# Optimization experiments

Measured on AMD Instinct MI355X. Metric: run time of the kernel, lower is better.

## Reference

```python
import jax, jax.numpy as jnp
import numpy as np
from jax import lax

B, C, H, W = 4, 256, 32, 32   # latent: NCHW, C == codebook embed dim
N_CODES = 16384


def setup_inputs() -> dict:
    key = jax.random.key(0)
    k1, k2, k3 = jax.random.split(key, 3)
    latent = jax.random.normal(k1, (B, C, H, W), jnp.float32)
    codebook = jax.random.normal(k2, (N_CODES, C), jnp.float32)
    dec_w = jax.random.normal(k3, (3, C, 3, 3), jnp.float32) * 0.02
    dec_b = jnp.zeros((3,), jnp.float32)
    return {"latent": latent, "codebook": codebook, "dec_w": dec_w, "dec_b": dec_b}


def vector_quantize(x, codebook):
    # x: [B,H,W,D], codebook: [N,D]. Squared-L2 nearest neighbor + gather,
    # straight-through gradient (replace_grad(x_q, x)).
    d = ((x * x).sum(-1, keepdims=True)
         - 2.0 * jnp.einsum('bhwd,nd->bhwn', x, codebook)
         + (codebook * codebook).sum(-1))          # [B,H,W,N]
    idx = jnp.argmin(d, axis=-1)                    # [B,H,W]
    x_q = codebook[idx]                             # gather -> [B,H,W,D]
    return x + lax.stop_gradient(x_q - x)


@jax.custom_vjp
def clamp_with_grad(x):
    return jnp.clip(x, 0.0, 1.0)

def _cwg_fwd(x):
    return jnp.clip(x, 0.0, 1.0), x

def _cwg_bwd(x, g):
    # pass gradient only where it points back toward the valid range
    keep = (g * (x - jnp.clip(x, 0.0, 1.0)) >= 0).astype(g.dtype)
    return (g * keep,)

clamp_with_grad.defvjp(_cwg_fwd, _cwg_bwd)


def decode(quant, dec_w, dec_b):
    # stub VQGAN decoder: single 3x3 conv embed_dim -> 3 (NCHW)
    y = lax.conv_general_dilated(quant, dec_w, window_strides=(1, 1),
                                 padding='SAME',
                                 dimension_numbers=('NCHW', 'OIHW', 'NCHW'))
    return y + dec_b[None, :, None, None]


def reference(latent, codebook, dec_w, dec_b):
    x = jnp.moveaxis(latent, 1, 3)                  # NCHW -> NHWC
    quant = jnp.moveaxis(vector_quantize(x, codebook), 3, 1)  # back to NCHW
    img = decode(quant, dec_w, dec_b)
    return clamp_with_grad((img + 1.0) * 0.5)
```

## Files before the change

kernel.cpp:

```cpp
#include <hip/hip_runtime.h>
#include <hip/hip_bf16.h>
#include <stdint.h>

#define P_TOT   4096
#define N_CODE  16384
#define DIM     256
#define HW      1024
#define CHW     262144
#define NBLK    64

typedef unsigned long long u64;
typedef unsigned short u16;
typedef __attribute__((ext_vector_type(4))) float f32x4;
typedef __attribute__((ext_vector_type(8))) short bf16x8;
typedef __attribute__((ext_vector_type(8))) unsigned short ushort8;

#define FENCE() asm volatile("" ::: "memory")
#define BAR()   __builtin_amdgcn_s_barrier()
#define VM(n)   asm volatile("s_waitcnt vmcnt(" #n ")" ::: "memory")

__device__ __forceinline__ unsigned int mono(float f) {
  unsigned int u = __float_as_uint(f);
  return (u & 0x80000000u) ? ~u : (u | 0x80000000u);
}
__device__ __forceinline__ u16 f2bf(float f) {
  __hip_bfloat16 h = __float2bfloat16(f);
  return *(u16*)&h;
}
__device__ __forceinline__ float bf2f(u16 b) {
  __hip_bfloat16 h = *(__hip_bfloat16*)&b;
  return __bfloat162float(h);
}
__device__ __forceinline__ void gload16(const void* g, void* l) {
  __builtin_amdgcn_global_load_lds(
      (const __attribute__((address_space(1))) unsigned int*)g,
      (__attribute__((address_space(3))) unsigned int*)l, 16, 0, 0);
}

__global__ __launch_bounds__(256) void k_split_cb(const float* __restrict__ cb,
                                                  u16* __restrict__ bfrag) {
  __shared__ float ls[64][68];
  int blk = blockIdx.x;
  int kp = blk & 3, bq = (blk >> 2) & 3, nb = blk >> 4;
  int t = threadIdx.x;
  int code0 = nb * 256 + bq * 64;
  int k0 = kp * 64;
  int lr = t >> 4, lc = (t & 15) * 4;
  #pragma unroll
  for (int pss = 0; pss < 4; ++pss) {
    int row = pss * 16 + lr;
    float4 v = *(const float4*)&cb[(size_t)(code0 + row) * DIM + k0 + lc];
    ls[row][lc] = v.x; ls[row][lc + 1] = v.y; ls[row][lc + 2] = v.z; ls[row][lc + 3] = v.w;
  }
  __syncthreads();
  int row64 = t & 63, g = t >> 6;
  #pragma unroll
  for (int it = 0; it < 4; ++it) {
    int combo = it * 4 + g;
    int kt2 = combo >> 3, s = (combo >> 1) & 3, h = combo & 1;
    int kt = kp * 2 + kt2;
    ushort8 o;
    #pragma unroll
    for (int e = 0; e < 8; ++e) {
      float x = ls[row64][kt2 * 32 + s * 8 + e];
      u16 hi = f2bf(x);
      o[e] = h ? f2bf(x - bf2f(hi)) : hi;
    }
    size_t unitIdx = (size_t)(nb * 8 + kt) * 4 + bq;
    *(ushort8*)&bfrag[unitIdx * 4096 + (size_t)((h * 4 + s) * 64 + row64) * 8] = o;
  }
}

__global__ __launch_bounds__(256) void k_split_x(const float* __restrict__ latent,
                                                 u16* __restrict__ xfrag) {
  __shared__ float ls[256][68];
  int blk = blockIdx.x;
  int aq = blk & 3, mb = blk >> 2;
  int t = threadIdx.x;
  int gp0 = mb * 256 + aq * 64;
  int b = gp0 >> 10, hw0 = gp0 & 1023;
  int hw = t & 63, cg = t >> 6;
  for (int pss = 0; pss < 64; ++pss) {
    int c = pss * 4 + cg;
    ls[c][hw] = latent[(size_t)b * CHW + (size_t)c * HW + hw0 + hw];
  }
  __syncthreads();
  int row64 = t & 63, g = t >> 6;
  #pragma unroll
  for (int it = 0; it < 16; ++it) {
    int combo = it * 4 + g;
    int kt = combo >> 3, s = (combo >> 1) & 3, h = combo & 1;
    ushort8 o;
    #pragma unroll
    for (int e = 0; e < 8; ++e) {
      float x = ls[kt * 32 + s * 8 + e][row64];
      u16 hi = f2bf(x);
      o[e] = h ? f2bf(x - bf2f(hi)) : hi;
    }
    size_t unitIdx = (size_t)(mb * 8 + kt) * 4 + aq;
    *(ushort8*)&xfrag[unitIdx * 4096 + (size_t)((h * 4 + s) * 64 + row64) * 8] = o;
  }
}

__global__ __launch_bounds__(256) void k_cnorm(const float* __restrict__ cb,
                                               float* __restrict__ cnorm) {
  int code = blockIdx.x * 4 + (threadIdx.x >> 6);
  int lane = threadIdx.x & 63;
  float4 v = ((const float4*)(cb + (size_t)code * DIM))[lane];
  float s = fmaf(v.x, v.x, fmaf(v.y, v.y, fmaf(v.z, v.z, v.w * v.w)));
  #pragma unroll
  for (int off = 32; off; off >>= 1) s += __shfl_down(s, off, 64);
  if (lane == 0) cnorm[code] = s;
}

__global__ __launch_bounds__(256) void k_wt(const float* __restrict__ w,
                                            float* __restrict__ wt) {
  int e = blockIdx.x * 256 + threadIdx.x;
  int ic = e & 255;
  int r = e >> 8;
  int kx = r % 3; r /= 3;
  int ky = r % 3;
  int oc = r / 3;
  wt[e] = w[((oc * 256 + ic) * 3 + ky) * 3 + kx];
}

__global__ __launch_bounds__(512, 2) void k_vq(const u16* __restrict__ xfrag,
                                               const u16* __restrict__ bfrag,
                                               const float* __restrict__ cnorm,
                                               u64* __restrict__ partial) {
  __shared__ u16 lds[2][2][4][4096];

  int bid = blockIdx.x;
  int wg = (bid & 7) * 128 + (bid >> 3);
  int nb = wg >> 4;
  int mb = wg & 15;

  int tid = threadIdx.x;
  int lane = tid & 63, w = tid >> 6;
  int fr = lane & 15, s = lane >> 4;
  int aq = w >> 1;
  int rbase = (w & 1) * 32;
  int tid8 = tid * 8;

  const u16* Xb = xfrag + (size_t)mb * 32 * 4096;
  const u16* Bb = bfrag + (size_t)nb * 32 * 4096;

  f32x4 acc[2][16] = {};
  bf16x8 ah[2], al[2], bh[4], bl[4];

  #pragma unroll
  for (int r = 0; r < 4; ++r) gload16(Xb + (size_t)r * 4096 + tid8, &lds[0][0][r][0] + tid8);
  #pragma unroll
  for (int r = 0; r < 4; ++r) gload16(Bb + (size_t)r * 4096 + tid8, &lds[0][1][r][0] + tid8);
  VM(3);
  BAR(); FENCE();

  #define READ_A(LA)                                                          \
    _Pragma("unroll")                                                         \
    for (int m = 0; m < 2; ++m) {                                             \
      ah[m] = *(const bf16x8*)&(LA)[aq * 4096 + (size_t)((0 + s) * 64 + rbase + m * 16 + fr) * 8]; \
      al[m] = *(const bf16x8*)&(LA)[aq * 4096 + (size_t)((4 + s) * 64 + rbase + m * 16 + fr) * 8]; \
    }
  #define READ_B(LB, q)                                                       \
    _Pragma("unroll")                                                         \
    for (int j = 0; j < 4; ++j) {                                             \
      bh[j] = *(const bf16x8*)&(LB)[(q) * 4096 + (size_t)((0 + s) * 64 + j * 16 + fr) * 8]; \
      bl[j] = *(const bf16x8*)&(LB)[(q) * 4096 + (size_t)((4 + s) * 64 + j * 16 + fr) * 8]; \
    }
  #define MFMAQ(q)                                                            \
    __builtin_amdgcn_s_setprio(1);                                            \
    _Pragma("unroll")                                                         \
    for (int m = 0; m < 2; ++m) {                                             \
      _Pragma("unroll")                                                       \
      for (int j = 0; j < 4; ++j)                                             \
        acc[m][(q) * 4 + j] = __builtin_amdgcn_mfma_f32_16x16x32_bf16(ah[m], bh[j], acc[m][(q) * 4 + j], 0, 0, 0); \
    }                                                                         \
    _Pragma("unroll")                                                         \
    for (int m = 0; m < 2; ++m) {                                             \
      _Pragma("unroll")                                                       \
      for (int j = 0; j < 4; ++j)                                             \
        acc[m][(q) * 4 + j] = __builtin_amdgcn_mfma_f32_16x16x32_bf16(ah[m], bl[j], acc[m][(q) * 4 + j], 0, 0, 0); \
    }                                                                         \
    _Pragma("unroll")                                                         \
    for (int m = 0; m < 2; ++m) {                                             \
      _Pragma("unroll")                                                       \
      for (int j = 0; j < 4; ++j)                                             \
        acc[m][(q) * 4 + j] = __builtin_amdgcn_mfma_f32_16x16x32_bf16(al[m], bh[j], acc[m][(q) * 4 + j], 0, 0, 0); \
    }                                                                         \
    __builtin_amdgcn_s_setprio(0);

  for (int t = 0; t < 7; ++t) {
    const int cur = t & 1, nxt = cur ^ 1;
    u16* LA = &lds[cur][0][0][0];
    u16* LB = &lds[cur][1][0][0];
    const size_t u1 = (size_t)(t + 1) * 4;
    READ_A(LA); READ_B(LB, 0);
    gload16(Xb + (u1 + 0) * 4096 + tid8, &lds[nxt][0][0][0] + tid8);
    gload16(Xb + (u1 + 1) * 4096 + tid8, &lds[nxt][0][1][0] + tid8);
    BAR();
    MFMAQ(0);
    VM(4); BAR(); FENCE();
    READ_B(LB, 1);
    gload16(Xb + (u1 + 2) * 4096 + tid8, &lds[nxt][0][2][0] + tid8);
    gload16(Xb + (u1 + 3) * 4096 + tid8, &lds[nxt][0][3][0] + tid8);
    BAR();
    MFMAQ(1);
    VM(5); BAR(); FENCE();
    READ_B(LB, 2);
    gload16(Bb + (u1 + 0) * 4096 + tid8, &lds[nxt][1][0][0] + tid8);
    gload16(Bb + (u1 + 1) * 4096 + tid8, &lds[nxt][1][1][0] + tid8);
    BAR();
    MFMAQ(2);
    VM(6); BAR(); FENCE();
    READ_B(LB, 3);
    gload16(Bb + (u1 + 2) * 4096 + tid8, &lds[nxt][1][2][0] + tid8);
    gload16(Bb + (u1 + 3) * 4096 + tid8, &lds[nxt][1][3][0] + tid8);
    BAR();
    MFMAQ(3);
    VM(3); BAR(); FENCE();
  }
  {
    u16* LA = &lds[1][0][0][0];
    u16* LB = &lds[1][1][0][0];
    READ_A(LA); READ_B(LB, 0);
    BAR(); MFMAQ(0); VM(2); BAR(); FENCE();
    READ_B(LB, 1);
    BAR(); MFMAQ(1); VM(1); BAR(); FENCE();
    READ_B(LB, 2);
    BAR(); MFMAQ(2); VM(0); BAR(); FENCE();
    READ_B(LB, 3);
    BAR(); MFMAQ(3);
  }

  float cnr[16];
  #pragma unroll
  for (int n = 0; n < 16; ++n) cnr[n] = cnorm[nb * 256 + n * 16 + fr];

  #pragma unroll
  for (int m = 0; m < 2; ++m) {
    u64 best[4];
    #pragma unroll
    for (int r = 0; r < 4; ++r) best[r] = ~0ull;
    #pragma unroll
    for (int n = 0; n < 16; ++n) {
      unsigned code = (unsigned)(nb * 256 + n * 16 + fr);
      #pragma unroll
      for (int r = 0; r < 4; ++r) {
        float val = fmaf(-2.0f, acc[m][n][r], cnr[n]);
        u64 key = ((u64)mono(val) << 32) | code;
        if (key < best[r]) best[r] = key;
      }
    }
    #pragma unroll
    for (int d = 1; d < 16; d <<= 1) {
      #pragma unroll
      for (int r = 0; r < 4; ++r) {
        u64 o = __shfl_xor(best[r], d, 64);
        if (o < best[r]) best[r] = o;
      }
    }
    if (fr == 0) {
      int rowb = mb * 256 + w * 32 + m * 16 + s * 4;
      #pragma unroll
      for (int r = 0; r < 4; ++r)
        partial[(size_t)(rowb + r) * NBLK + nb] = best[r];
    }
  }
}

__global__ __launch_bounds__(64) void k_reduce(const u64* __restrict__ partial,
                                               const float* __restrict__ latent,
                                               const float* __restrict__ cb,
                                               int* __restrict__ idxo) {
  int p = blockIdx.x;
  int t = threadIdx.x;
  u64 v = partial[(size_t)p * NBLK + t];
  u64 m1 = v;
  #pragma unroll
  for (int d = 1; d < 64; d <<= 1) { u64 o = __shfl_xor(m1, d, 64); if (o < m1) m1 = o; }
  u64 vv = (v == m1) ? ~0ull : v;
  u64 m2 = vv;
  #pragma unroll
  for (int d = 1; d < 64; d <<= 1) { u64 o = __shfl_xor(m2, d, 64); if (o < m2) m2 = o; }
  int n1 = (int)(m1 & 0xFFFFFFFFull);
  int n2 = (int)(m2 & 0xFFFFFFFFull);

  int b = p >> 10, hw = p & 1023;
  const float* xb = latent + (size_t)b * CHW + hw;
  double d1 = 0.0, d2 = 0.0;
  #pragma unroll
  for (int q = 0; q < 4; ++q) {
    int c = t * 4 + q;
    double xv = (double)xb[(size_t)c * HW];
    double e1 = xv - (double)cb[(size_t)n1 * DIM + c]; d1 += e1 * e1;
    double e2 = xv - (double)cb[(size_t)n2 * DIM + c]; d2 += e2 * e2;
  }
  #pragma unroll
  for (int d = 32; d; d >>= 1) {
    d1 += __shfl_down(d1, d, 64);
    d2 += __shfl_down(d2, d, 64);
  }
  if (t == 0) {
    idxo[p] = (d2 < d1 || (d2 == d1 && n2 < n1)) ? n2 : n1;
  }
}

__global__ __launch_bounds__(256) void k_conv(const float* __restrict__ cb,
                                              const int* __restrict__ idx,
                                              const float* __restrict__ wt,
                                              const float* __restrict__ bias,
                                              float* __restrict__ out) {
  int y = blockIdx.x, b = blockIdx.y;
  int t = threadIdx.x;
  int x = t & 31, icg = t >> 5;
  float a0 = 0.f, a1 = 0.f, a2 = 0.f;
  #pragma unroll
  for (int dy = -1; dy <= 1; dy++) {
    int yy = y + dy;
    if (yy < 0 || yy >= 32) continue;
    #pragma unroll
    for (int dx = -1; dx <= 1; dx++) {
      int xx = x + dx;
      if (xx < 0 || xx >= 32) continue;
      int n = idx[b * HW + yy * 32 + xx];
      const float4* crow = (const float4*)(cb + (size_t)n * DIM + icg * 32);
      int tap = (dy + 1) * 3 + (dx + 1);
      const float4* w0 = (const float4*)(wt + (size_t)(0 * 9 + tap) * DIM + icg * 32);
      const float4* w1 = (const float4*)(wt + (size_t)(1 * 9 + tap) * DIM + icg * 32);
      const float4* w2 = (const float4*)(wt + (size_t)(2 * 9 + tap) * DIM + icg * 32);
      #pragma unroll
      for (int q = 0; q < 8; q++) {
        float4 qv = crow[q];
        float4 wa = w0[q];
        a0 = fmaf(qv.x, wa.x, a0); a0 = fmaf(qv.y, wa.y, a0);
        a0 = fmaf(qv.z, wa.z, a0); a0 = fmaf(qv.w, wa.w, a0);
        float4 wb = w1[q];
        a1 = fmaf(qv.x, wb.x, a1); a1 = fmaf(qv.y, wb.y, a1);
        a1 = fmaf(qv.z, wb.z, a1); a1 = fmaf(qv.w, wb.w, a1);
        float4 wcv = w2[q];
        a2 = fmaf(qv.x, wcv.x, a2); a2 = fmaf(qv.y, wcv.y, a2);
        a2 = fmaf(qv.z, wcv.z, a2); a2 = fmaf(qv.w, wcv.w, a2);
      }
    }
  }
  __shared__ float red[3][32][8];
  red[0][x][icg] = a0; red[1][x][icg] = a1; red[2][x][icg] = a2;
  __syncthreads();
  if (t < 96) {
    int oc = t >> 5, xo = t & 31;
    float sum = 0.f;
    #pragma unroll
    for (int k = 0; k < 8; k++) sum += red[oc][xo][k];
    sum += bias[oc];
    sum = (sum + 1.0f) * 0.5f;
    sum = fminf(fmaxf(sum, 0.0f), 1.0f);
    out[((size_t)(b * 3 + oc) * 32 + y) * 32 + xo] = sum;
  }
}

extern "C" void kernel_launch(void* const* d_in, const int* in_sizes, int n_in,
                              void* d_out, int out_size, void* d_ws, size_t ws_size,
                              hipStream_t stream) {
  const float* latent = (const float*)d_in[0];
  const float* cb     = (const float*)d_in[1];
  const float* dec_w  = (const float*)d_in[2];
  const float* dec_b  = (const float*)d_in[3];
  float* out = (float*)d_out;

  char* ws = (char*)d_ws;
  u64*   partial = (u64*)ws;
  float* cnorm   = (float*)(ws + 0x200000);
  int*   idx     = (int*)  (ws + 0x210000);
  float* wt      = (float*)(ws + 0x214000);
  u16*   xfrag   = (u16*)  (ws + 0x400000);
  u16*   bfrag   = (u16*)  (ws + 0x800000);

  k_split_cb<<<dim3(1024), dim3(256), 0, stream>>>(cb, bfrag);
  k_split_x <<<dim3(64),   dim3(256), 0, stream>>>(latent, xfrag);
  k_cnorm   <<<dim3(N_CODE / 4), dim3(256), 0, stream>>>(cb, cnorm);
  k_wt      <<<dim3(27),   dim3(256), 0, stream>>>(dec_w, wt);
  k_vq      <<<dim3(1024), dim3(512), 0, stream>>>(xfrag, bfrag, cnorm, partial);
  k_reduce  <<<dim3(P_TOT), dim3(64), 0, stream>>>(partial, latent, cb, idx);
  k_conv    <<<dim3(32, 4), dim3(256), 0, stream>>>(cb, idx, wt, dec_b, out);
}
```

Before: 203.7 us.

## Hold X fragments in registers, stream codebook only, and merge prep kernels

```diff
diff --git a/kernel.cpp b/kernel.cpp
--- a/kernel.cpp
+++ b/kernel.cpp
@@ -7,7 +7,7 @@
 #define DIM     256
 #define HW      1024
 #define CHW     262144
-#define NBLK    64
+#define NBLK    16
 
 typedef unsigned long long u64;
 typedef unsigned short u16;
@@ -37,234 +37,219 @@
       (__attribute__((address_space(3))) unsigned int*)l, 16, 0, 0);
 }
 
-__global__ __launch_bounds__(256) void k_split_cb(const float* __restrict__ cb,
-                                                  u16* __restrict__ bfrag) {
+__global__ __launch_bounds__(256) void k_prep(const float* __restrict__ cb,
+                                              const float* __restrict__ latent,
+                                              const float* __restrict__ dec_w,
+                                              u16* __restrict__ bfrag,
+                                              u16* __restrict__ xfrag,
+                                              float* __restrict__ cnorm,
+                                              float* __restrict__ wt) {
   __shared__ float ls[64][68];
-  int blk = blockIdx.x;
-  int kp = blk & 3, bq = (blk >> 2) & 3, nb = blk >> 4;
+  int bid = blockIdx.x;
   int t = threadIdx.x;
-  int code0 = nb * 256 + bq * 64;
-  int k0 = kp * 64;
-  int lr = t >> 4, lc = (t & 15) * 4;
-  #pragma unroll
-  for (int pss = 0; pss < 4; ++pss) {
-    int row = pss * 16 + lr;
-    float4 v = *(const float4*)&cb[(size_t)(code0 + row) * DIM + k0 + lc];
-    ls[row][lc] = v.x; ls[row][lc + 1] = v.y; ls[row][lc + 2] = v.z; ls[row][lc + 3] = v.w;
-  }
-  __syncthreads();
-  int row64 = t & 63, g = t >> 6;
-  #pragma unroll
-  for (int it = 0; it < 4; ++it) {
-    int combo = it * 4 + g;
-    int kt2 = combo >> 3, s = (combo >> 1) & 3, h = combo & 1;
-    int kt = kp * 2 + kt2;
-    ushort8 o;
-    #pragma unroll
-    for (int e = 0; e < 8; ++e) {
-      float x = ls[row64][kt2 * 32 + s * 8 + e];
-      u16 hi = f2bf(x);
-      o[e] = h ? f2bf(x - bf2f(hi)) : hi;
-    }
-    size_t unitIdx = (size_t)(nb * 8 + kt) * 4 + bq;
-    *(ushort8*)&bfrag[unitIdx * 4096 + (size_t)((h * 4 + s) * 64 + row64) * 8] = o;
-  }
-}
-
-__global__ __launch_bounds__(256) void k_split_x(const float* __restrict__ latent,
-                                                 u16* __restrict__ xfrag) {
-  __shared__ float ls[256][68];
-  int blk = blockIdx.x;
-  int aq = blk & 3, mb = blk >> 2;
-  int t = threadIdx.x;
-  int gp0 = mb * 256 + aq * 64;
-  int b = gp0 >> 10, hw0 = gp0 & 1023;
-  int hw = t & 63, cg = t >> 6;
-  for (int pss = 0; pss < 64; ++pss) {
-    int c = pss * 4 + cg;
-    ls[c][hw] = latent[(size_t)b * CHW + (size_t)c * HW + hw0 + hw];
-  }
-  __syncthreads();
-  int row64 = t & 63, g = t >> 6;
-  #pragma unroll
-  for (int it = 0; it < 16; ++it) {
-    int combo = it * 4 + g;
-    int kt = combo >> 3, s = (combo >> 1) & 3, h = combo & 1;
-    ushort8 o;
-    #pragma unroll
-    for (int e = 0; e < 8; ++e) {
-      float x = ls[kt * 32 + s * 8 + e][row64];
-      u16 hi = f2bf(x);
-      o[e] = h ? f2bf(x - bf2f(hi)) : hi;
-    }
-    size_t unitIdx = (size_t)(mb * 8 + kt) * 4 + aq;
-    *(ushort8*)&xfrag[unitIdx * 4096 + (size_t)((h * 4 + s) * 64 + row64) * 8] = o;
-  }
-}
-
-__global__ __launch_bounds__(256) void k_cnorm(const float* __restrict__ cb,
-                                               float* __restrict__ cnorm) {
-  int code = blockIdx.x * 4 + (threadIdx.x >> 6);
-  int lane = threadIdx.x & 63;
-  float4 v = ((const float4*)(cb + (size_t)code * DIM))[lane];
-  float s = fmaf(v.x, v.x, fmaf(v.y, v.y, fmaf(v.z, v.z, v.w * v.w)));
-  #pragma unroll
-  for (int off = 32; off; off >>= 1) s += __shfl_down(s, off, 64);
-  if (lane == 0) cnorm[code] = s;
-}
-
-__global__ __launch_bounds__(256) void k_wt(const float* __restrict__ w,
-                                            float* __restrict__ wt) {
-  int e = blockIdx.x * 256 + threadIdx.x;
-  int ic = e & 255;
-  int r = e >> 8;
-  int kx = r % 3; r /= 3;
-  int ky = r % 3;
-  int oc = r / 3;
-  wt[e] = w[((oc * 256 + ic) * 3 + ky) * 3 + kx];
-}
-
-__global__ __launch_bounds__(512, 2) void k_vq(const u16* __restrict__ xfrag,
+  if (bid < 1024) {
+    int blk = bid;
+    int kp = blk & 3, bq = (blk >> 2) & 3, nb = blk >> 4;
+    int code0 = nb * 256 + bq * 64;
+    int k0 = kp * 64;
+    int lr = t >> 4, lc = (t & 15) * 4;
+    #pragma unroll
+    for (int pss = 0; pss < 4; ++pss) {
+      int row = pss * 16 + lr;
+      float4 v = *(const float4*)&cb[(size_t)(code0 + row) * DIM + k0 + lc];
+      ls[row][lc] = v.x; ls[row][lc + 1] = v.y; ls[row][lc + 2] = v.z; ls[row][lc + 3] = v.w;
+    }
+    __syncthreads();
+    int row64 = t & 63, g = t >> 6;
+    #pragma unroll
+    for (int it = 0; it < 4; ++it) {
+      int combo = it * 4 + g;
+      int kt2 = combo >> 3, s = (combo >> 1) & 3, h = combo & 1;
+      int kt = kp * 2 + kt2;
+      ushort8 o;
+      #pragma unroll
+      for (int e = 0; e < 8; ++e) {
+        float x = ls[row64][kt2 * 32 + s * 8 + e];
+        u16 hi = f2bf(x);
+        o[e] = h ? f2bf(x - bf2f(hi)) : hi;
+      }
+      size_t unitIdx = (size_t)(nb * 8 + kt) * 4 + bq;
+      *(ushort8*)&bfrag[unitIdx * 4096 + (size_t)((h * 4 + s) * 64 + row64) * 8] = o;
+    }
+  } else if (bid < 1280) {
+    int blk = bid - 1024;
+    int kp = blk & 3, rowblk = blk >> 2;
+    int g0 = rowblk * 64;
+    int b = g0 >> 10, hw0 = g0 & 1023;
+    int c0 = kp * 64;
+    int ch = t >> 4, px4 = (t & 15) * 4;
+    #pragma unroll
+    for (int pss = 0; pss < 4; ++pss) {
+      int c = pss * 16 + ch;
+      float4 v = *(const float4*)&latent[(size_t)b * CHW + (size_t)(c0 + c) * HW + hw0 + px4];
+      ls[px4 + 0][c] = v.x; ls[px4 + 1][c] = v.y; ls[px4 + 2][c] = v.z; ls[px4 + 3][c] = v.w;
+    }
+    __syncthreads();
+    int row64 = t & 63, g = t >> 6;
+    #pragma unroll
+    for (int it = 0; it < 4; ++it) {
+      int combo = it * 4 + g;
+      int kt2 = combo >> 3, s = (combo >> 1) & 3, h = combo & 1;
+      int kt = kp * 2 + kt2;
+      ushort8 o;
+      #pragma unroll
+      for (int e = 0; e < 8; ++e) {
+        float x = ls[row64][kt2 * 32 + s * 8 + e];
+        u16 hi = f2bf(x);
+        o[e] = h ? f2bf(x - bf2f(hi)) : hi;
+      }
+      int mbO = rowblk >> 2, aq = rowblk & 3;
+      size_t unitIdx = (size_t)(mbO * 8 + kt) * 4 + aq;
+      *(ushort8*)&xfrag[unitIdx * 4096 + (size_t)((h * 4 + s) * 64 + row64) * 8] = o;
+    }
+  } else if (bid < 5376) {
+    int code = (bid - 1280) * 4 + (t >> 6);
+    int lane = t & 63;
+    float4 v = ((const float4*)(cb + (size_t)code * DIM))[lane];
+    float sv = fmaf(v.x, v.x, fmaf(v.y, v.y, fmaf(v.z, v.z, v.w * v.w)));
+    #pragma unroll
+    for (int off = 32; off; off >>= 1) sv += __shfl_down(sv, off, 64);
+    if (lane == 0) cnorm[code] = sv;
+  } else {
+    int e = (bid - 5376) * 256 + t;
+    if (e < 6912) {
+      int ic = e & 255; int r = e >> 8;
+      int kx = r % 3; r /= 3; int ky = r % 3; int oc = r / 3;
+      wt[e] = dec_w[((oc * 256 + ic) * 3 + ky) * 3 + kx];
+    }
+  }
+}
+
+__global__ __launch_bounds__(512, 4) void k_vq(const u16* __restrict__ xfrag,
                                                const u16* __restrict__ bfrag,
                                                const float* __restrict__ cnorm,
                                                u64* __restrict__ partial) {
-  __shared__ u16 lds[2][2][4][4096];
+  __shared__ u16 bbuf[2][4][4096];
+  __shared__ float cnl[1024];
 
   int bid = blockIdx.x;
-  int wg = (bid & 7) * 128 + (bid >> 3);
-  int nb = wg >> 4;
-  int mb = wg & 15;
-
-  int tid = threadIdx.x;
-  int lane = tid & 63, w = tid >> 6;
+  int xcd = bid & 7, ix = bid >> 3;
+  int nbc = xcd * 2 + (ix >> 5);
+  int mb  = ix & 31;
+
+  int tid = threadIdx.x, lane = tid & 63, w = tid >> 6;
   int fr = lane & 15, s = lane >> 4;
-  int aq = w >> 1;
-  int rbase = (w & 1) * 32;
   int tid8 = tid * 8;
 
-  const u16* Xb = xfrag + (size_t)mb * 32 * 4096;
-  const u16* Bb = bfrag + (size_t)nb * 32 * 4096;
-
-  f32x4 acc[2][16] = {};
-  bf16x8 ah[2], al[2], bh[4], bl[4];
-
-  #pragma unroll
-  for (int r = 0; r < 4; ++r) gload16(Xb + (size_t)r * 4096 + tid8, &lds[0][0][r][0] + tid8);
-  #pragma unroll
-  for (int r = 0; r < 4; ++r) gload16(Bb + (size_t)r * 4096 + tid8, &lds[0][1][r][0] + tid8);
-  VM(3);
-  BAR(); FENCE();
-
-  #define READ_A(LA)                                                          \
-    _Pragma("unroll")                                                         \
-    for (int m = 0; m < 2; ++m) {                                             \
-      ah[m] = *(const bf16x8*)&(LA)[aq * 4096 + (size_t)((0 + s) * 64 + rbase + m * 16 + fr) * 8]; \
-      al[m] = *(const bf16x8*)&(LA)[aq * 4096 + (size_t)((4 + s) * 64 + rbase + m * 16 + fr) * 8]; \
-    }
-  #define READ_B(LB, q)                                                       \
-    _Pragma("unroll")                                                         \
-    for (int j = 0; j < 4; ++j) {                                             \
-      bh[j] = *(const bf16x8*)&(LB)[(q) * 4096 + (size_t)((0 + s) * 64 + j * 16 + fr) * 8]; \
-      bl[j] = *(const bf16x8*)&(LB)[(q) * 4096 + (size_t)((4 + s) * 64 + j * 16 + fr) * 8]; \
-    }
-  #define MFMAQ(q)                                                            \
+  const u16* Bb = bfrag + (size_t)nbc * 32 * 16384;
+
+  #pragma unroll
+  for (int r = 0; r < 4; ++r)
+    gload16(Bb + (size_t)r * 4096 + tid8, &bbuf[0][r][0] + tid8);
+
+  int rowg = mb * 128 + w * 16;
+  int mbO = rowg >> 8, aq = (rowg >> 6) & 3, rb = rowg & 63;
+  bf16x8 ah[8], al[8];
+  #pragma unroll
+  for (int kt = 0; kt < 8; ++kt) {
+    const u16* ub = xfrag + ((size_t)(mbO * 8 + kt) * 4 + aq) * 4096;
+    ah[kt] = *(const bf16x8*)&ub[(size_t)((0 + s) * 64 + rb + fr) * 8];
+    al[kt] = *(const bf16x8*)&ub[(size_t)((4 + s) * 64 + rb + fr) * 8];
+  }
+  cnl[tid]       = cnorm[nbc * 1024 + tid];
+  cnl[tid + 512] = cnorm[nbc * 1024 + 512 + tid];
+  __syncthreads();
+
+  f32x4 acc[16] = {};
+  u64 best[4] = {~0ull, ~0ull, ~0ull, ~0ull};
+  bf16x8 bh[8], bl[8];
+
+  #define READ8(buf, half)                                                    \
+    _Pragma("unroll")                                                         \
+    for (int j = 0; j < 8; ++j) {                                             \
+      const int jj = (half) * 8 + j;                                          \
+      const u16* bp = &bbuf[buf][jj >> 2][0];                                 \
+      bh[j] = *(const bf16x8*)&bp[(size_t)((0 + s) * 64 + (jj & 3) * 16 + fr) * 8]; \
+      bl[j] = *(const bf16x8*)&bp[(size_t)((4 + s) * 64 + (jj & 3) * 16 + fr) * 8]; \
+    }
+  #define MFMA8(kt, half)                                                     \
     __builtin_amdgcn_s_setprio(1);                                            \
     _Pragma("unroll")                                                         \
-    for (int m = 0; m < 2; ++m) {                                             \
+    for (int j = 0; j < 8; ++j)                                               \
+      acc[(half) * 8 + j] = __builtin_amdgcn_mfma_f32_16x16x32_bf16(ah[kt], bh[j], acc[(half) * 8 + j], 0, 0, 0); \
+    _Pragma("unroll")                                                         \
+    for (int j = 0; j < 8; ++j)                                               \
+      acc[(half) * 8 + j] = __builtin_amdgcn_mfma_f32_16x16x32_bf16(ah[kt], bl[j], acc[(half) * 8 + j], 0, 0, 0); \
+    _Pragma("unroll")                                                         \
+    for (int j = 0; j < 8; ++j)                                               \
+      acc[(half) * 8 + j] = __builtin_amdgcn_mfma_f32_16x16x32_bf16(al[kt], bh[j], acc[(half) * 8 + j], 0, 0, 0); \
+    __builtin_amdgcn_s_setprio(0);
+  #define STAGE2(nxt, base, u0)                                               \
+    gload16((base) + (size_t)(u0) * 4096 + tid8, &bbuf[nxt][(u0)][0] + tid8); \
+    gload16((base) + (size_t)((u0) + 1) * 4096 + tid8, &bbuf[nxt][(u0) + 1][0] + tid8);
+  #define FOLD(pp)                                                            \
+    _Pragma("unroll")                                                         \
+    for (int jj = 0; jj < 16; ++jj) {                                         \
+      float cnv = cnl[(pp) * 256 + jj * 16 + fr];                             \
+      unsigned code = (unsigned)(nbc * 1024 + (pp) * 256 + jj * 16 + fr);     \
       _Pragma("unroll")                                                       \
-      for (int j = 0; j < 4; ++j)                                             \
-        acc[m][(q) * 4 + j] = __builtin_amdgcn_mfma_f32_16x16x32_bf16(ah[m], bh[j], acc[m][(q) * 4 + j], 0, 0, 0); \
-    }                                                                         \
-    _Pragma("unroll")                                                         \
-    for (int m = 0; m < 2; ++m) {                                             \
-      _Pragma("unroll")                                                       \
-      for (int j = 0; j < 4; ++j)                                             \
-        acc[m][(q) * 4 + j] = __builtin_amdgcn_mfma_f32_16x16x32_bf16(ah[m], bl[j], acc[m][(q) * 4 + j], 0, 0, 0); \
-    }                                                                         \
-    _Pragma("unroll")                                                         \
-    for (int m = 0; m < 2; ++m) {                                             \
-      _Pragma("unroll")                                                       \
-      for (int j = 0; j < 4; ++j)                                             \
-        acc[m][(q) * 4 + j] = __builtin_amdgcn_mfma_f32_16x16x32_bf16(al[m], bh[j], acc[m][(q) * 4 + j], 0, 0, 0); \
-    }                                                                         \
-    __builtin_amdgcn_s_setprio(0);
-
-  for (int t = 0; t < 7; ++t) {
-    const int cur = t & 1, nxt = cur ^ 1;
-    u16* LA = &lds[cur][0][0][0];
-    u16* LB = &lds[cur][1][0][0];
-    const size_t u1 = (size_t)(t + 1) * 4;
-    READ_A(LA); READ_B(LB, 0);
-    gload16(Xb + (u1 + 0) * 4096 + tid8, &lds[nxt][0][0][0] + tid8);
-    gload16(Xb + (u1 + 1) * 4096 + tid8, &lds[nxt][0][1][0] + tid8);
-    BAR();
-    MFMAQ(0);
-    VM(4); BAR(); FENCE();
-    READ_B(LB, 1);
-    gload16(Xb + (u1 + 2) * 4096 + tid8, &lds[nxt][0][2][0] + tid8);
-    gload16(Xb + (u1 + 3) * 4096 + tid8, &lds[nxt][0][3][0] + tid8);
-    BAR();
-    MFMAQ(1);
-    VM(5); BAR(); FENCE();
-    READ_B(LB, 2);
-    gload16(Bb + (u1 + 0) * 4096 + tid8, &lds[nxt][1][0][0] + tid8);
-    gload16(Bb + (u1 + 1) * 4096 + tid8, &lds[nxt][1][1][0] + tid8);
-    BAR();
-    MFMAQ(2);
-    VM(6); BAR(); FENCE();
-    READ_B(LB, 3);
-    gload16(Bb + (u1 + 2) * 4096 + tid8, &lds[nxt][1][2][0] + tid8);
-    gload16(Bb + (u1 + 3) * 4096 + tid8, &lds[nxt][1][3][0] + tid8);
-    BAR();
-    MFMAQ(3);
-    VM(3); BAR(); FENCE();
-  }
-  {
-    u16* LA = &lds[1][0][0][0];
-    u16* LB = &lds[1][1][0][0];
-    READ_A(LA); READ_B(LB, 0);
-    BAR(); MFMAQ(0); VM(2); BAR(); FENCE();
-    READ_B(LB, 1);
-    BAR(); MFMAQ(1); VM(1); BAR(); FENCE();
-    READ_B(LB, 2);
-    BAR(); MFMAQ(2); VM(0); BAR(); FENCE();
-    READ_B(LB, 3);
-    BAR(); MFMAQ(3);
-  }
-
-  float cnr[16];
-  #pragma unroll
-  for (int n = 0; n < 16; ++n) cnr[n] = cnorm[nb * 256 + n * 16 + fr];
-
-  #pragma unroll
-  for (int m = 0; m < 2; ++m) {
-    u64 best[4];
-    #pragma unroll
-    for (int r = 0; r < 4; ++r) best[r] = ~0ull;
-    #pragma unroll
-    for (int n = 0; n < 16; ++n) {
-      unsigned code = (unsigned)(nb * 256 + n * 16 + fr);
-      #pragma unroll
-      for (int r = 0; r < 4; ++r) {
-        float val = fmaf(-2.0f, acc[m][n][r], cnr[n]);
-        u64 key = ((u64)mono(val) << 32) | code;
-        if (key < best[r]) best[r] = key;
+      for (int r = 0; r < 4; ++r) {                                           \
+        float val = fmaf(-2.0f, acc[jj][r], cnv);                             \
+        u64 key = ((u64)mono(val) << 32) | code;                              \
+        if (key < best[r]) best[r] = key;                                     \
+        acc[jj][r] = 0.0f;                                                    \
+      }                                                                       \
+    }
+
+  #pragma unroll 1
+  for (int p = 0; p < 4; ++p) {
+    #pragma unroll
+    for (int kt = 0; kt < 8; ++kt) {
+      const int cur = kt & 1, nxt = cur ^ 1;
+      const u16* SB = Bb + (size_t)(p * 8 + kt + 1) * 16384;
+      if (kt < 7) {
+        READ8(cur, 0);
+        STAGE2(nxt, SB, 0);
+        BAR();
+        MFMA8(kt, 0);
+        VM(2); BAR(); FENCE();
+        READ8(cur, 1);
+        STAGE2(nxt, SB, 2);
+        BAR();
+        MFMA8(kt, 1);
+        VM(2); BAR(); FENCE();
+      } else {
+        bool last = (p == 3);
+        READ8(cur, 0);
+        if (!last) { STAGE2(nxt, SB, 0); }
+        BAR();
+        MFMA8(kt, 0);
+        if (!last) { VM(2); } else { VM(0); }
+        BAR(); FENCE();
+        READ8(cur, 1);
+        if (!last) { STAGE2(nxt, SB, 2); }
+        BAR();
+        MFMA8(kt, 1);
+        FOLD(p);
+        if (!last) { VM(2); }
+        BAR(); FENCE();
       }
     }
-    #pragma unroll
-    for (int d = 1; d < 16; d <<= 1) {
-      #pragma unroll
-      for (int r = 0; r < 4; ++r) {
-        u64 o = __shfl_xor(best[r], d, 64);
-        if (o < best[r]) best[r] = o;
-      }
-    }
-    if (fr == 0) {
-      int rowb = mb * 256 + w * 32 + m * 16 + s * 4;
-      #pragma unroll
-      for (int r = 0; r < 4; ++r)
-        partial[(size_t)(rowb + r) * NBLK + nb] = best[r];
-    }
+  }
+
+  #pragma unroll
+  for (int d = 1; d < 16; d <<= 1) {
+    #pragma unroll
+    for (int r = 0; r < 4; ++r) {
+      u64 o = __shfl_xor(best[r], d, 64);
+      if (o < best[r]) best[r] = o;
+    }
+  }
+  if (fr == 0) {
+    int rowb = mb * 128 + w * 16 + s * 4;
+    #pragma unroll
+    for (int r = 0; r < 4; ++r)
+      partial[(size_t)(rowb + r) * NBLK + nbc] = best[r];
   }
 }
 
@@ -274,7 +259,7 @@
                                                int* __restrict__ idxo) {
   int p = blockIdx.x;
   int t = threadIdx.x;
-  u64 v = partial[(size_t)p * NBLK + t];
+  u64 v = (t < NBLK) ? partial[(size_t)p * NBLK + t] : ~0ull;
   u64 m1 = v;
   #pragma unroll
   for (int d = 1; d < 64; d <<= 1) { u64 o = __shfl_xor(m1, d, 64); if (o < m1) m1 = o; }
@@ -369,17 +354,14 @@
 
   char* ws = (char*)d_ws;
   u64*   partial = (u64*)ws;
-  float* cnorm   = (float*)(ws + 0x200000);
-  int*   idx     = (int*)  (ws + 0x210000);
-  float* wt      = (float*)(ws + 0x214000);
-  u16*   xfrag   = (u16*)  (ws + 0x400000);
+  float* cnorm   = (float*)(ws + 0x080000);
+  int*   idx     = (int*)  (ws + 0x090000);
+  float* wt      = (float*)(ws + 0x094000);
+  u16*   xfrag   = (u16*)  (ws + 0x100000);
   u16*   bfrag   = (u16*)  (ws + 0x800000);
 
-  k_split_cb<<<dim3(1024), dim3(256), 0, stream>>>(cb, bfrag);
-  k_split_x <<<dim3(64),   dim3(256), 0, stream>>>(latent, xfrag);
-  k_cnorm   <<<dim3(N_CODE / 4), dim3(256), 0, stream>>>(cb, cnorm);
-  k_wt      <<<dim3(27),   dim3(256), 0, stream>>>(dec_w, wt);
-  k_vq      <<<dim3(1024), dim3(512), 0, stream>>>(xfrag, bfrag, cnorm, partial);
-  k_reduce  <<<dim3(P_TOT), dim3(64), 0, stream>>>(partial, latent, cb, idx);
-  k_conv    <<<dim3(32, 4), dim3(256), 0, stream>>>(cb, idx, wt, dec_b, out);
-}
+  k_prep  <<<dim3(5403), dim3(256), 0, stream>>>(cb, latent, dec_w, bfrag, xfrag, cnorm, wt);
+  k_vq    <<<dim3(512),  dim3(512), 0, stream>>>(xfrag, bfrag, cnorm, partial);
+  k_reduce<<<dim3(P_TOT), dim3(64), 0, stream>>>(partial, latent, cb, idx);
+  k_conv  <<<dim3(32, 4), dim3(256), 0, stream>>>(cb, idx, wt, dec_b, out);
+}
```

Result: slower. 430.4 us (+111.3%).
